# Kernel optimization log

Measured on AMD Instinct MI355X. Metric: run time of the kernel, lower is better.

The kernel has to match this reference:

```python
import jax, jax.numpy as jnp
import numpy as np

NEG_INF = -10000000000.0
HEADS = 16


def setup_inputs() -> dict:
    key = jax.random.key(0)
    ks = jax.random.split(key, 12)
    B, S, E = 2, 2048, 1024
    sc = 1.0 / np.sqrt(E)
    inp = {
        "input_queries": jax.random.normal(ks[0], (B, S, E), jnp.float32),
        "input_keys": jax.random.normal(ks[1], (B, S, E), jnp.float32),
        "input_values": jax.random.normal(ks[2], (B, S, E), jnp.float32),
        # causal mask: True where attention is disallowed (masked_fill where mask==True)
        "mask": jnp.triu(jnp.ones((S, S), jnp.bool_), k=1)[None, None],
        "Wq": jax.random.normal(ks[3], (E, E), jnp.float32) * sc,
        "bq": jax.random.normal(ks[4], (E,), jnp.float32) * 0.01,
        "Wk": jax.random.normal(ks[5], (E, E), jnp.float32) * sc,
        "bk": jax.random.normal(ks[6], (E,), jnp.float32) * 0.01,
        "Wv": jax.random.normal(ks[7], (E, E), jnp.float32) * sc,
        "bv": jax.random.normal(ks[8], (E,), jnp.float32) * 0.01,
        "Wo": jax.random.normal(ks[9], (E, E), jnp.float32) * sc,
        "bo": jax.random.normal(ks[10], (E,), jnp.float32) * 0.01,
    }
    return inp


def reference(input_queries, input_keys, input_values, mask, Wq, bq, Wk, bk, Wv, bv, Wo, bo):
    B, S, E = input_queries.shape
    H = HEADS
    D = E // H
    # torch Linear: y = x @ W.T + b
    q = (input_queries @ Wq.T + bq).reshape(B, S, H, D).transpose(0, 2, 1, 3)  # bhsd
    k = (input_keys @ Wk.T + bk).reshape(B, S, H, D).transpose(0, 2, 1, 3)
    v = (input_values @ Wv.T + bv).reshape(B, S, H, D).transpose(0, 2, 1, 3)
    scores = jnp.einsum('bhqd,bhkd->bhqk', q, k) / jnp.sqrt(jnp.asarray(D, q.dtype))
    scores = jnp.where(mask, jnp.asarray(NEG_INF, scores.dtype), scores)
    attn = jax.nn.softmax(scores, axis=-1)
    out = jnp.einsum('bhqk,bhkd->bhqd', attn, v).transpose(0, 2, 1, 3).reshape(B, S, E)
    return out @ Wo.T + bo
```

## Files before the change

kernel.cpp:

```cpp
#include <hip/hip_runtime.h>
#include <hip/hip_bf16.h>

#define DEVI __device__ __forceinline__

using bf16x8 = __attribute__((ext_vector_type(8))) short;
using f32x4  = __attribute__((ext_vector_type(4))) float;
using f32x16 = __attribute__((ext_vector_type(16))) float;

#define LOG2E 1.4426950408889634f

DEVI unsigned short f2bf(float f){
  unsigned int u = __float_as_uint(f);
  return (unsigned short)((u + 0x7fffu + ((u>>16)&1u)) >> 16);
}

DEVI unsigned int cvt_pk_bf16(float lo, float hi){
  unsigned int r;
  asm("v_cvt_pk_bf16_f32 %0, %1, %2" : "=v"(r) : "v"(lo), "v"(hi));
  return r;
}

#if __has_builtin(__builtin_amdgcn_exp2f)
#define EXP2(x) __builtin_amdgcn_exp2f(x)
#else
#define EXP2(x) exp2f(x)
#endif

DEVI void gload_lds16(const unsigned short* src, unsigned short* lds){
  __builtin_amdgcn_global_load_lds((const __attribute__((address_space(1))) void*)src,
                                   (__attribute__((address_space(3))) void*)lds, 16, 0, 0);
}

DEVI bf16x8 mk8(unsigned w0, unsigned w1, unsigned w2, unsigned w3){
  union { unsigned u[4]; bf16x8 v; } x;
  x.u[0]=w0; x.u[1]=w1; x.u[2]=w2; x.u[3]=w3;
  return x.v;
}

__global__ __launch_bounds__(256) void convert_kernel(
  const float* __restrict__ Xq, const float* __restrict__ Xk, const float* __restrict__ Xv,
  const float* __restrict__ Wq, const float* __restrict__ Wk, const float* __restrict__ Wv,
  const float* __restrict__ Wo, unsigned short* __restrict__ ws)
{
  const int y = blockIdx.y;
  const float* src;
  unsigned short* dst;
  int n4;
  if (y < 3){
    src = (y==0)?Xq:((y==1)?Xk:Xv);
    dst = ws + (size_t)y*4194304;
    n4 = 1048576;
  } else {
    src = (y==3)?Wq:((y==4)?Wk:((y==5)?Wv:Wo));
    dst = ws + 12582912 + (size_t)(y-3)*1048576;
    n4 = 262144;
  }
  const int stride = gridDim.x * 256;
  for (int i = blockIdx.x*256 + threadIdx.x; i < n4; i += stride){
    float4 v = ((const float4*)src)[i];
    uint2 u;
    u.x = cvt_pk_bf16(v.x, v.y);
    u.y = cvt_pk_bf16(v.z, v.w);
    ((uint2*)dst)[i] = u;
  }
}

__global__ __launch_bounds__(256, 3) void proj_qkv_kernel(
  const unsigned short* __restrict__ Xb, const unsigned short* __restrict__ Wb,
  const float* __restrict__ Bq, const float* __restrict__ Bk, const float* __restrict__ Bv,
  unsigned short* __restrict__ Qo, unsigned short* __restrict__ Ko, unsigned short* __restrict__ Vo)
{
  const int L = blockIdx.x;
  const int xcd = L & 7, g = L >> 3;
  const int combo = xcd*12 + (g>>3);
  const int tn = g & 7;
  const int p  = combo >> 5;
  const int tm = combo & 31;

  const unsigned short* __restrict__ A = Xb + (size_t)p*4194304;
  const unsigned short* __restrict__ B = Wb + (size_t)p*1048576;
  const float* __restrict__ Bb = (p==0)?Bq:((p==1)?Bk:Bv);
  unsigned short* __restrict__ Out = (p==0)?Qo:((p==1)?Ko:Vo);
  const float oscale = (p==0)?(0.125f*LOG2E):1.0f;

  const int m0 = tm*128, n0 = tn*128;
  const int tid = threadIdx.x;
  const int w = tid>>6, l = tid&63;
  const int wr = w>>1, wc = w&1;
  const int lg = l>>4, lr = l&15;

  __shared__ unsigned short As[3][4096];
  __shared__ unsigned short Bs[3][4096];

  f32x4 acc[4][4];
  #pragma unroll
  for (int i=0;i<4;i++)
    #pragma unroll
    for (int j=0;j<4;j++){ f32x4 z = {0.f,0.f,0.f,0.f}; acc[i][j] = z; }

  const int srow = l>>2;
  const int schk = (l&3) ^ (srow&3);
  auto stage = [&](int h, int buf){
    const int kt = h*32;
    #pragma unroll
    for (int i=0;i<2;i++){
      int rbase = w*32 + i*16;
      gload_lds16(A + (size_t)(m0+rbase+srow)*1024 + kt + schk*8, &As[buf][0] + rbase*32);
      gload_lds16(B + (size_t)(n0+rbase+srow)*1024 + kt + schk*8, &Bs[buf][0] + rbase*32);
    }
  };

  stage(0, 0);
  stage(1, 1);

  const int sca = (lg ^ (lr&3)) << 4;
  int cur = 0;
  for (int h=0; h<32; ++h){
    if (h < 31) asm volatile("s_waitcnt vmcnt(4)" ::: "memory");
    else        asm volatile("s_waitcnt vmcnt(0)" ::: "memory");
    __builtin_amdgcn_s_barrier();
    __builtin_amdgcn_sched_barrier(0);
    if (h < 30){
      int nb = cur + 2; if (nb >= 3) nb -= 3;
      stage(h+2, nb);
    }

    bf16x8 af[4], bfr[4];
    #pragma unroll
    for (int f=0;f<4;f++){
      af[f]  = *(const bf16x8*)((const char*)&As[cur][0] + (wr*64 + f*16 + lr)*64 + sca);
      bfr[f] = *(const bf16x8*)((const char*)&Bs[cur][0] + (wc*64 + f*16 + lr)*64 + sca);
    }
    #pragma unroll
    for (int fr=0;fr<4;fr++)
      #pragma unroll
      for (int fc=0;fc<4;fc++)
        acc[fr][fc] = __builtin_amdgcn_mfma_f32_16x16x32_bf16(af[fr], bfr[fc], acc[fr][fc], 0,0,0);

    cur = (cur==2) ? 0 : cur+1;
  }

  if (p == 2){
    #pragma unroll
    for (int fc=0;fc<4;fc++){
      int n = n0 + wc*64 + fc*16 + lr;
      float bias = Bb[n];
      int h = n>>6, d = n&63;
      #pragma unroll
      for (int fr=0;fr<4;fr++){
        int m = m0 + wr*64 + fr*16 + lg*4;
        int b = m>>11, s = m & 2047;
        uint2 u;
        u.x = cvt_pk_bf16(acc[fr][fc][0]+bias, acc[fr][fc][1]+bias);
        u.y = cvt_pk_bf16(acc[fr][fc][2]+bias, acc[fr][fc][3]+bias);
        *(uint2*)(Out + (((size_t)((b<<4)+h)*64 + d)*2048 + s)) = u;
      }
    }
  } else {
    #pragma unroll
    for (int fc=0;fc<4;fc++){
      int n = n0 + wc*64 + fc*16 + lr;
      float bias = Bb[n];
      int h = n>>6, d = n&63;
      #pragma unroll
      for (int fr=0;fr<4;fr++){
        #pragma unroll
        for (int r=0;r<4;r++){
          int m = m0 + wr*64 + fr*16 + lg*4 + r;
          int b = m>>11, s = m & 2047;
          float v = (acc[fr][fc][r] + bias) * oscale;
          Out[ ((size_t)((b<<4)+h)*2048 + (size_t)s)*64 + d ] = f2bf(v);
        }
      }
    }
  }
}

__global__ __launch_bounds__(256,2) void attn_kernel(
  const unsigned short* __restrict__ Q, const unsigned short* __restrict__ Kg,
  const unsigned short* __restrict__ Vt, unsigned short* __restrict__ AO)
{
  const int idx = blockIdx.x;
  const int qt = 15 - (idx >> 5);
  const int bh = idx & 31;
  const size_t base = (size_t)bh * 131072;
  const int q0 = qt * 128;
  const int tid = threadIdx.x, w = tid>>6, l = tid&63;
  const int lq = l & 31, hi = l >> 5;
  const int qq = q0 + w*32 + lq;

  __shared__ unsigned short Ks[2][4096];
  __shared__ unsigned short Vs[2][4096];

  bf16x8 qf[4];
  {
    const unsigned short* qp = Q + base + (size_t)qq*64;
    #pragma unroll
    for (int s=0;s<4;s++) qf[s] = *(const bf16x8*)(qp + s*16 + hi*8);
  }

  f32x16 oacc[2];
  #pragma unroll
  for (int dt=0;dt<2;dt++)
    #pragma unroll
    for (int r=0;r<16;r++) oacc[dt][r] = 0.f;
  float m_i = -INFINITY, l_i = 0.f;

  const int NT = 2*qt + 2;

  auto stage = [&](int kt, int half){
    const int kv0 = kt*64;
    #pragma unroll
    for (int i=0;i<2;i++){
      int c = tid + i*256;
      int row = c>>3;
      int kc = (c&7) ^ (row&7);
      gload_lds16(Kg + base + (size_t)(kv0+row)*64 + kc*8, &Ks[half][0] + c*8);
      gload_lds16(Vt + base + (size_t)row*2048 + kv0 + kc*8, &Vs[half][0] + c*8);
    }
  };

  stage(0, 0);
  __syncthreads();

  for (int kt=0; kt<NT; kt++){
    const int cur = kt & 1;
    if (kt+1 < NT) stage(kt+1, cur^1);
    const int kv0 = kt*64;

    f32x16 sacc[2];
    #pragma unroll
    for (int kvt=0;kvt<2;kvt++)
      #pragma unroll
      for (int r=0;r<16;r++) sacc[kvt][r] = 0.f;

    __builtin_amdgcn_s_setprio(1);
    #pragma unroll
    for (int kvt=0;kvt<2;kvt++){
      int row = kvt*32 + lq;
      const char* kb = (const char*)&Ks[cur][0] + row*128;
      int swz = (row&7)<<4;
      #pragma unroll
      for (int s=0;s<4;s++){
        bf16x8 kf = *(const bf16x8*)(kb + ((s*32 + hi*16) ^ swz));
        sacc[kvt] = __builtin_amdgcn_mfma_f32_32x32x16_bf16(kf, qf[s], sacc[kvt], 0,0,0);
      }
    }
    __builtin_amdgcn_s_setprio(0);

    #pragma unroll
    for (int kvt=0;kvt<2;kvt++){
      if (kv0 + kvt*32 + 31 > q0 + w*32){
        #pragma unroll
        for (int r=0;r<16;r++){
          int kvv = kv0 + kvt*32 + (r&3) + 8*(r>>2) + 4*hi;
          if (kvv > qq) sacc[kvt][r] = -1e30f;
        }
      }
    }

    float mt = sacc[0][0];
    #pragma unroll
    for (int kvt=0;kvt<2;kvt++)
      #pragma unroll
      for (int r=0;r<16;r++) mt = fmaxf(mt, sacc[kvt][r]);
    mt = fmaxf(mt, __shfl_xor(mt, 32));

    if (__any(mt > m_i + 8.f)){
      float mn = fmaxf(m_i, mt);
      float sc = EXP2(m_i - mn);
      m_i = mn;
      l_i *= sc;
      #pragma unroll
      for (int dt=0;dt<2;dt++)
        #pragma unroll
        for (int r=0;r<16;r++) oacc[dt][r] *= sc;
    }
    float rs = 0.f;
    #pragma unroll
    for (int kvt=0;kvt<2;kvt++)
      #pragma unroll
      for (int r=0;r<16;r++){
        float pv = EXP2(sacc[kvt][r] - m_i);
        sacc[kvt][r] = pv;
        rs += pv;
      }
    rs += __shfl_xor(rs, 32);
    l_i += rs;

    unsigned pa[8], pb[8], sa[8], sb[8];
    #pragma unroll
    for (int g=0; g<8; g++){
      int kvt = g>>2, gl = g&3;
      pa[g] = cvt_pk_bf16(sacc[kvt][4*gl+0], sacc[kvt][4*gl+1]);
      pb[g] = cvt_pk_bf16(sacc[kvt][4*gl+2], sacc[kvt][4*gl+3]);
      sa[g] = __shfl_xor(pa[g], 32);
      sb[g] = __shfl_xor(pb[g], 32);
    }
    bf16x8 pfrag[4];
    #pragma unroll
    for (int s=0;s<4;s++){
      int g0 = (s>>1)*4 + 2*(s&1);
      unsigned w0 = hi ? sa[g0+1] : pa[g0];
      unsigned w1 = hi ? sb[g0+1] : pb[g0];
      unsigned w2 = hi ? pa[g0+1] : sa[g0];
      unsigned w3 = hi ? pb[g0+1] : sb[g0];
      pfrag[s] = mk8(w0, w1, w2, w3);
    }

    __builtin_amdgcn_s_setprio(1);
    #pragma unroll
    for (int dt=0;dt<2;dt++){
      int row = dt*32 + lq;
      const char* vb = (const char*)&Vs[cur][0] + row*128;
      int swz = (row&7)<<4;
      #pragma unroll
      for (int s=0;s<4;s++){
        bf16x8 vf = *(const bf16x8*)(vb + ((s*32 + hi*16) ^ swz));
        oacc[dt] = __builtin_amdgcn_mfma_f32_32x32x16_bf16(vf, pfrag[s], oacc[dt], 0,0,0);
      }
    }
    __builtin_amdgcn_s_setprio(0);

    __syncthreads();
  }

  unsigned short* Es = &Ks[0][0] + w*2048;
  float inv = 1.0f / l_i;
  {
    char* eb = (char*)Es + lq*128;
    int swz = (lq&7)<<4;
    #pragma unroll
    for (int dt=0;dt<2;dt++)
      #pragma unroll
      for (int g=0;g<4;g++){
        int d0 = dt*32 + 8*g + 4*hi;
        unsigned u0 = cvt_pk_bf16(oacc[dt][4*g+0]*inv, oacc[dt][4*g+1]*inv);
        unsigned u1 = cvt_pk_bf16(oacc[dt][4*g+2]*inv, oacc[dt][4*g+3]*inv);
        *(unsigned*)(eb + ((d0*2    ) ^ swz)) = u0;
        *(unsigned*)(eb + ((d0*2 + 4) ^ swz)) = u1;
      }
  }
  const int b = bh>>4, h = bh&15;
  {
    const char* rb = (const char*)Es + lq*128;
    int swz = (lq&7)<<4;
    unsigned short* op = AO + ((size_t)b*2048 + (q0 + w*32 + lq))*1024 + h*64 + hi*32;
    #pragma unroll
    for (int j=0;j<2;j++){
      bf16x8 v = *(const bf16x8*)(rb + ((hi*64 + j*16) ^ swz));
      *(bf16x8*)(op + j*8) = v;
    }
    #pragma unroll
    for (int j=2;j<4;j++){
      bf16x8 v = *(const bf16x8*)(rb + ((hi*64 + j*16) ^ swz));
      *(bf16x8*)(op + j*8) = v;
    }
  }
}

__global__ __launch_bounds__(256, 3) void proj_out_kernel(
  const unsigned short* __restrict__ A, const unsigned short* __restrict__ B,
  const float* __restrict__ Bb, float* __restrict__ Out)
{
  const int L = blockIdx.x;
  const int xcd = L & 7, g = L >> 3;
  const int tm = xcd*4 + (g>>3);
  const int tn = g & 7;
  const int m0 = tm*128, n0 = tn*128;
  const int tid = threadIdx.x;
  const int w = tid>>6, l = tid&63;
  const int wr = w>>1, wc = w&1;
  const int lg = l>>4, lr = l&15;

  __shared__ unsigned short As[3][4096];
  __shared__ unsigned short Bs[3][4096];

  f32x4 acc[4][4];
  #pragma unroll
  for (int i=0;i<4;i++)
    #pragma unroll
    for (int j=0;j<4;j++){ f32x4 z = {0.f,0.f,0.f,0.f}; acc[i][j] = z; }

  const int srow = l>>2;
  const int schk = (l&3) ^ (srow&3);
  auto stage = [&](int h, int buf){
    const int kt = h*32;
    #pragma unroll
    for (int i=0;i<2;i++){
      int rbase = w*32 + i*16;
      gload_lds16(A + (size_t)(m0+rbase+srow)*1024 + kt + schk*8, &As[buf][0] + rbase*32);
      gload_lds16(B + (size_t)(n0+rbase+srow)*1024 + kt + schk*8, &Bs[buf][0] + rbase*32);
    }
  };

  stage(0, 0);
  stage(1, 1);

  const int sca = (lg ^ (lr&3)) << 4;
  int cur = 0;
  for (int h=0; h<32; ++h){
    if (h < 31) asm volatile("s_waitcnt vmcnt(4)" ::: "memory");
    else        asm volatile("s_waitcnt vmcnt(0)" ::: "memory");
    __builtin_amdgcn_s_barrier();
    __builtin_amdgcn_sched_barrier(0);
    if (h < 30){
      int nb = cur + 2; if (nb >= 3) nb -= 3;
      stage(h+2, nb);
    }

    bf16x8 af[4], bfr[4];
    #pragma unroll
    for (int f=0;f<4;f++){
      af[f]  = *(const bf16x8*)((const char*)&As[cur][0] + (wr*64 + f*16 + lr)*64 + sca);
      bfr[f] = *(const bf16x8*)((const char*)&Bs[cur][0] + (wc*64 + f*16 + lr)*64 + sca);
    }
    #pragma unroll
    for (int fr=0;fr<4;fr++)
      #pragma unroll
      for (int fc=0;fc<4;fc++)
        acc[fr][fc] = __builtin_amdgcn_mfma_f32_16x16x32_bf16(af[fr], bfr[fc], acc[fr][fc], 0,0,0);

    cur = (cur==2) ? 0 : cur+1;
  }

  #pragma unroll
  for (int fc=0;fc<4;fc++){
    int n = n0 + wc*64 + fc*16 + lr;
    float bias = Bb[n];
    #pragma unroll
    for (int fr=0;fr<4;fr++){
      #pragma unroll
      for (int r=0;r<4;r++){
        int m = m0 + wr*64 + fr*16 + lg*4 + r;
        Out[(size_t)m*1024 + n] = acc[fr][fc][r] + bias;
      }
    }
  }
}

extern "C" void kernel_launch(void* const* d_in, const int* in_sizes, int n_in,
                              void* d_out, int out_size, void* d_ws, size_t ws_size,
                              hipStream_t stream)
{
  const float* Xq = (const float*)d_in[0];
  const float* Xk = (const float*)d_in[1];
  const float* Xv = (const float*)d_in[2];
  const float* Wq = (const float*)d_in[4];
  const float* bq = (const float*)d_in[5];
  const float* Wk = (const float*)d_in[6];
  const float* bk = (const float*)d_in[7];
  const float* Wv = (const float*)d_in[8];
  const float* bv = (const float*)d_in[9];
  const float* Wo = (const float*)d_in[10];
  const float* bo = (const float*)d_in[11];

  unsigned short* ws  = (unsigned short*)d_ws;
  unsigned short* Xb  = ws;
  unsigned short* Wb  = ws + 12582912;
  unsigned short* Qw  = ws + 16777216;
  unsigned short* Kw  = ws + 20971520;
  unsigned short* Vw  = ws + 25165824;
  unsigned short* AOw = ws + 29360128;
  float* out = (float*)d_out;

  convert_kernel<<<dim3(512,7), 256, 0, stream>>>(Xq,Xk,Xv,Wq,Wk,Wv,Wo, ws);
  proj_qkv_kernel<<<768, 256, 0, stream>>>(Xb, Wb, bq,bk,bv, Qw,Kw,Vw);
  attn_kernel<<<512, 256, 0, stream>>>(Qw,Kw,Vw,AOw);
  proj_out_kernel<<<256, 256, 0, stream>>>(AOw, Wb + 3*1048576, bo, out);
}
```

Measured before the change: 235.5 us.

## Pair causal query tiles per block and map heads to XCDs in attention

The attention kernel moves from 256-thread blocks on 128-row query tiles to 128-thread blocks that each handle two 64-row query tiles, a long one (31-pr) and a short one (pr). This evens out the causal workload across blocks. Each group of four heads is kept on one XCD so K/V reuse stays in that XCD's L2. The cost is fewer waves per block, more staging loads per thread, and a serial second phase inside each block.

```diff
diff --git a/kernel.cpp b/kernel.cpp
--- a/kernel.cpp
+++ b/kernel.cpp
@@ -176,43 +176,27 @@
   }
 }
 
-__global__ __launch_bounds__(256,2) void attn_kernel(
+__global__ __launch_bounds__(128, 2) void attn_kernel(
   const unsigned short* __restrict__ Q, const unsigned short* __restrict__ Kg,
   const unsigned short* __restrict__ Vt, unsigned short* __restrict__ AO)
 {
   const int idx = blockIdx.x;
-  const int qt = 15 - (idx >> 5);
-  const int bh = idx & 31;
+  const int xcd = idx & 7, j = idx >> 3;
+  const int bh = 4*xcd + (j & 3);
+  const int pr = j >> 2;
   const size_t base = (size_t)bh * 131072;
-  const int q0 = qt * 128;
   const int tid = threadIdx.x, w = tid>>6, l = tid&63;
   const int lq = l & 31, hi = l >> 5;
-  const int qq = q0 + w*32 + lq;
+  const int b = bh>>4, hh = bh&15;
 
   __shared__ unsigned short Ks[2][4096];
   __shared__ unsigned short Vs[2][4096];
 
-  bf16x8 qf[4];
-  {
-    const unsigned short* qp = Q + base + (size_t)qq*64;
-    #pragma unroll
-    for (int s=0;s<4;s++) qf[s] = *(const bf16x8*)(qp + s*16 + hi*8);
-  }
-
-  f32x16 oacc[2];
-  #pragma unroll
-  for (int dt=0;dt<2;dt++)
-    #pragma unroll
-    for (int r=0;r<16;r++) oacc[dt][r] = 0.f;
-  float m_i = -INFINITY, l_i = 0.f;
-
-  const int NT = 2*qt + 2;
-
   auto stage = [&](int kt, int half){
     const int kv0 = kt*64;
     #pragma unroll
-    for (int i=0;i<2;i++){
-      int c = tid + i*256;
+    for (int i=0;i<4;i++){
+      int c = tid + i*128;
       int row = c>>3;
       int kc = (c&7) ^ (row&7);
       gload_lds16(Kg + base + (size_t)(kv0+row)*64 + kc*8, &Ks[half][0] + c*8);
@@ -220,141 +204,160 @@
     }
   };
 
-  stage(0, 0);
-  __syncthreads();
-
-  for (int kt=0; kt<NT; kt++){
-    const int cur = kt & 1;
-    if (kt+1 < NT) stage(kt+1, cur^1);
-    const int kv0 = kt*64;
-
-    f32x16 sacc[2];
-    #pragma unroll
-    for (int kvt=0;kvt<2;kvt++)
-      #pragma unroll
-      for (int r=0;r<16;r++) sacc[kvt][r] = 0.f;
-
-    __builtin_amdgcn_s_setprio(1);
-    #pragma unroll
-    for (int kvt=0;kvt<2;kvt++){
-      int row = kvt*32 + lq;
-      const char* kb = (const char*)&Ks[cur][0] + row*128;
-      int swz = (row&7)<<4;
+  #pragma unroll 1
+  for (int ph=0; ph<2; ph++){
+    const int t = ph ? pr : (31 - pr);
+    const int q0 = t*64;
+    const int qw0 = q0 + w*32;
+    const int qq = qw0 + lq;
+
+    bf16x8 qf[4];
+    {
+      const unsigned short* qp = Q + base + (size_t)qq*64;
+      #pragma unroll
+      for (int s=0;s<4;s++) qf[s] = *(const bf16x8*)(qp + s*16 + hi*8);
+    }
+
+    f32x16 oacc[2];
+    #pragma unroll
+    for (int dt=0;dt<2;dt++)
+      #pragma unroll
+      for (int r=0;r<16;r++) oacc[dt][r] = 0.f;
+    float m_i = -INFINITY, l_i = 0.f;
+
+    const int NT = t + 1;
+
+    __syncthreads();
+    stage(0, 0);
+    __syncthreads();
+
+    for (int kt=0; kt<NT; kt++){
+      const int cur = kt & 1;
+      if (kt+1 < NT) stage(kt+1, cur^1);
+      const int kv0 = kt*64;
+
+      f32x16 sacc[2];
+      #pragma unroll
+      for (int kvt=0;kvt<2;kvt++)
+        #pragma unroll
+        for (int r=0;r<16;r++) sacc[kvt][r] = 0.f;
+
+      __builtin_amdgcn_s_setprio(1);
+      #pragma unroll
+      for (int kvt=0;kvt<2;kvt++){
+        int row = kvt*32 + lq;
+        const char* kb = (const char*)&Ks[cur][0] + row*128;
+        int swz = (row&7)<<4;
+        #pragma unroll
+        for (int s=0;s<4;s++){
+          bf16x8 kf = *(const bf16x8*)(kb + ((s*32 + hi*16) ^ swz));
+          sacc[kvt] = __builtin_amdgcn_mfma_f32_32x32x16_bf16(kf, qf[s], sacc[kvt], 0,0,0);
+        }
+      }
+      __builtin_amdgcn_s_setprio(0);
+
+      #pragma unroll
+      for (int kvt=0;kvt<2;kvt++){
+        if (kv0 + kvt*32 + 31 > qw0){
+          #pragma unroll
+          for (int r=0;r<16;r++){
+            int kvv = kv0 + kvt*32 + (r&3) + 8*(r>>2) + 4*hi;
+            if (kvv > qq) sacc[kvt][r] = -1e30f;
+          }
+        }
+      }
+
+      float mt = sacc[0][0];
+      #pragma unroll
+      for (int kvt=0;kvt<2;kvt++)
+        #pragma unroll
+        for (int r=0;r<16;r++) mt = fmaxf(mt, sacc[kvt][r]);
+      mt = fmaxf(mt, __shfl_xor(mt, 32));
+
+      if (__any(mt > m_i + 8.f)){
+        float mn = fmaxf(m_i, mt);
+        float sc = EXP2(m_i - mn);
+        m_i = mn;
+        l_i *= sc;
+        #pragma unroll
+        for (int dt=0;dt<2;dt++)
+          #pragma unroll
+          for (int r=0;r<16;r++) oacc[dt][r] *= sc;
+      }
+      float rs = 0.f;
+      #pragma unroll
+      for (int kvt=0;kvt<2;kvt++)
+        #pragma unroll
+        for (int r=0;r<16;r++){
+          float pv = EXP2(sacc[kvt][r] - m_i);
+          sacc[kvt][r] = pv;
+          rs += pv;
+        }
+      rs += __shfl_xor(rs, 32);
+      l_i += rs;
+
+      unsigned pa[8], pb[8], sa[8], sb[8];
+      #pragma unroll
+      for (int g=0; g<8; g++){
+        int kvt = g>>2, gl = g&3;
+        pa[g] = cvt_pk_bf16(sacc[kvt][4*gl+0], sacc[kvt][4*gl+1]);
+        pb[g] = cvt_pk_bf16(sacc[kvt][4*gl+2], sacc[kvt][4*gl+3]);
+        sa[g] = __shfl_xor(pa[g], 32);
+        sb[g] = __shfl_xor(pb[g], 32);
+      }
+      bf16x8 pfrag[4];
       #pragma unroll
       for (int s=0;s<4;s++){
-        bf16x8 kf = *(const bf16x8*)(kb + ((s*32 + hi*16) ^ swz));
-        sacc[kvt] = __builtin_amdgcn_mfma_f32_32x32x16_bf16(kf, qf[s], sacc[kvt], 0,0,0);
-      }
-    }
-    __builtin_amdgcn_s_setprio(0);
-
-    #pragma unroll
-    for (int kvt=0;kvt<2;kvt++){
-      if (kv0 + kvt*32 + 31 > q0 + w*32){
-        #pragma unroll
-        for (int r=0;r<16;r++){
-          int kvv = kv0 + kvt*32 + (r&3) + 8*(r>>2) + 4*hi;
-          if (kvv > qq) sacc[kvt][r] = -1e30f;
-        }
-      }
-    }
-
-    float mt = sacc[0][0];
-    #pragma unroll
-    for (int kvt=0;kvt<2;kvt++)
-      #pragma unroll
-      for (int r=0;r<16;r++) mt = fmaxf(mt, sacc[kvt][r]);
-    mt = fmaxf(mt, __shfl_xor(mt, 32));
-
-    if (__any(mt > m_i + 8.f)){
-      float mn = fmaxf(m_i, mt);
-      float sc = EXP2(m_i - mn);
-      m_i = mn;
-      l_i *= sc;
+        int g0 = (s>>1)*4 + 2*(s&1);
+        unsigned w0 = hi ? sa[g0+1] : pa[g0];
+        unsigned w1 = hi ? sb[g0+1] : pb[g0];
+        unsigned w2 = hi ? pa[g0+1] : sa[g0];
+        unsigned w3 = hi ? pb[g0+1] : sb[g0];
+        pfrag[s] = mk8(w0, w1, w2, w3);
+      }
+
+      __builtin_amdgcn_s_setprio(1);
+      #pragma unroll
+      for (int dt=0;dt<2;dt++){
+        int row = dt*32 + lq;
+        const char* vb = (const char*)&Vs[cur][0] + row*128;
+        int swz = (row&7)<<4;
+        #pragma unroll
+        for (int s=0;s<4;s++){
+          bf16x8 vf = *(const bf16x8*)(vb + ((s*32 + hi*16) ^ swz));
+          oacc[dt] = __builtin_amdgcn_mfma_f32_32x32x16_bf16(vf, pfrag[s], oacc[dt], 0,0,0);
+        }
+      }
+      __builtin_amdgcn_s_setprio(0);
+
+      __syncthreads();
+    }
+
+    unsigned short* Es = &Ks[0][0] + w*2048;
+    float inv = 1.0f / l_i;
+    {
+      char* eb = (char*)Es + lq*128;
+      int swz = (lq&7)<<4;
       #pragma unroll
       for (int dt=0;dt<2;dt++)
         #pragma unroll
-        for (int r=0;r<16;r++) oacc[dt][r] *= sc;
-    }
-    float rs = 0.f;
-    #pragma unroll
-    for (int kvt=0;kvt<2;kvt++)
-      #pragma unroll
-      for (int r=0;r<16;r++){
-        float pv = EXP2(sacc[kvt][r] - m_i);
-        sacc[kvt][r] = pv;
-        rs += pv;
-      }
-    rs += __shfl_xor(rs, 32);
-    l_i += rs;
-
-    unsigned pa[8], pb[8], sa[8], sb[8];
-    #pragma unroll
-    for (int g=0; g<8; g++){
-      int kvt = g>>2, gl = g&3;
-      pa[g] = cvt_pk_bf16(sacc[kvt][4*gl+0], sacc[kvt][4*gl+1]);
-      pb[g] = cvt_pk_bf16(sacc[kvt][4*gl+2], sacc[kvt][4*gl+3]);
-      sa[g] = __shfl_xor(pa[g], 32);
-      sb[g] = __shfl_xor(pb[g], 32);
-    }
-    bf16x8 pfrag[4];
-    #pragma unroll
-    for (int s=0;s<4;s++){
-      int g0 = (s>>1)*4 + 2*(s&1);
-      unsigned w0 = hi ? sa[g0+1] : pa[g0];
-      unsigned w1 = hi ? sb[g0+1] : pb[g0];
-      unsigned w2 = hi ? pa[g0+1] : sa[g0];
-      unsigned w3 = hi ? pb[g0+1] : sb[g0];
-      pfrag[s] = mk8(w0, w1, w2, w3);
-    }
-
-    __builtin_amdgcn_s_setprio(1);
-    #pragma unroll
-    for (int dt=0;dt<2;dt++){
-      int row = dt*32 + lq;
-      const char* vb = (const char*)&Vs[cur][0] + row*128;
-      int swz = (row&7)<<4;
-      #pragma unroll
-      for (int s=0;s<4;s++){
-        bf16x8 vf = *(const bf16x8*)(vb + ((s*32 + hi*16) ^ swz));
-        oacc[dt] = __builtin_amdgcn_mfma_f32_32x32x16_bf16(vf, pfrag[s], oacc[dt], 0,0,0);
-      }
-    }
-    __builtin_amdgcn_s_setprio(0);
-
-    __syncthreads();
-  }
-
-  unsigned short* Es = &Ks[0][0] + w*2048;
-  float inv = 1.0f / l_i;
-  {
-    char* eb = (char*)Es + lq*128;
-    int swz = (lq&7)<<4;
-    #pragma unroll
-    for (int dt=0;dt<2;dt++)
-      #pragma unroll
-      for (int g=0;g<4;g++){
-        int d0 = dt*32 + 8*g + 4*hi;
-        unsigned u0 = cvt_pk_bf16(oacc[dt][4*g+0]*inv, oacc[dt][4*g+1]*inv);
-        unsigned u1 = cvt_pk_bf16(oacc[dt][4*g+2]*inv, oacc[dt][4*g+3]*inv);
-        *(unsigned*)(eb + ((d0*2    ) ^ swz)) = u0;
-        *(unsigned*)(eb + ((d0*2 + 4) ^ swz)) = u1;
-      }
-  }
-  const int b = bh>>4, h = bh&15;
-  {
-    const char* rb = (const char*)Es + lq*128;
-    int swz = (lq&7)<<4;
-    unsigned short* op = AO + ((size_t)b*2048 + (q0 + w*32 + lq))*1024 + h*64 + hi*32;
-    #pragma unroll
-    for (int j=0;j<2;j++){
-      bf16x8 v = *(const bf16x8*)(rb + ((hi*64 + j*16) ^ swz));
-      *(bf16x8*)(op + j*8) = v;
-    }
-    #pragma unroll
-    for (int j=2;j<4;j++){
-      bf16x8 v = *(const bf16x8*)(rb + ((hi*64 + j*16) ^ swz));
-      *(bf16x8*)(op + j*8) = v;
+        for (int g=0;g<4;g++){
+          int d0 = dt*32 + 8*g + 4*hi;
+          unsigned u0 = cvt_pk_bf16(oacc[dt][4*g+0]*inv, oacc[dt][4*g+1]*inv);
+          unsigned u1 = cvt_pk_bf16(oacc[dt][4*g+2]*inv, oacc[dt][4*g+3]*inv);
+          *(unsigned*)(eb + ((d0*2    ) ^ swz)) = u0;
+          *(unsigned*)(eb + ((d0*2 + 4) ^ swz)) = u1;
+        }
+    }
+    {
+      const char* rb = (const char*)Es + lq*128;
+      int swz = (lq&7)<<4;
+      unsigned short* op = AO + ((size_t)b*2048 + qq)*1024 + hh*64 + hi*32;
+      #pragma unroll
+      for (int jj=0;jj<4;jj++){
+        bf16x8 v = *(const bf16x8*)(rb + ((hi*64 + jj*16) ^ swz));
+        *(bf16x8*)(op + jj*8) = v;
+      }
     }
   }
 }
@@ -466,6 +469,6 @@
 
   convert_kernel<<<dim3(512,7), 256, 0, stream>>>(Xq,Xk,Xv,Wq,Wk,Wv,Wo, ws);
   proj_qkv_kernel<<<768, 256, 0, stream>>>(Xb, Wb, bq,bk,bv, Qw,Kw,Vw);
-  attn_kernel<<<512, 256, 0, stream>>>(Qw,Kw,Vw,AOw);
+  attn_kernel<<<512, 128, 0, stream>>>(Qw,Kw,Vw,AOw);
   proj_out_kernel<<<256, 256, 0, stream>>>(AOw, Wb + 3*1048576, bo, out);
 }
```

Result: no change. 237.6 us (+0.9%).
